# Performance work log

Measured on AMD Instinct MI355X. Metric: run time of the kernel, lower is better.

## Reference

```python
import jax, jax.numpy as jnp
import numpy as np

N, D = 131072, 512
G, NG = 512, 256  # G groups of equal size NG, contiguous; N == G*NG
MARGIN, LAMBDA_CD, LAMBDA_CDD, LAMBDA_PCC, K_MARGIN = 2.0, 0.0, 1.0, 1.0, 0.02
EPS = 1e-6


def setup_inputs() -> dict:
    key = jax.random.key(0)
    k1, k2, k3, k4 = jax.random.split(key, 4)
    z_r = jax.random.normal(k1, (N, D), jnp.float32)
    z_r = z_r / jnp.linalg.norm(z_r, axis=-1, keepdims=True)
    z_v = jax.random.normal(k2, (N, D), jnp.float32)
    z_v = z_v / jnp.linalg.norm(z_v, axis=-1, keepdims=True)
    labels = jax.random.randint(k3, (N,), 0, 2)
    groups = jnp.repeat(jnp.arange(G), NG)  # contiguous equal-size groups
    var_lens = jax.random.randint(k4, (N,), 0, 10000)
    return {"z_r": z_r, "z_v": z_v, "labels": labels, "groups": groups, "var_lens": var_lens}


def reference(z_r, z_v, labels, groups, var_lens):
    # cosine distance per pair: [N]
    d = 1.0 - jnp.sum(z_r * z_v, axis=-1)

    mb = (labels == 0).astype(d.dtype)
    mp = (labels == 1).astype(d.dtype)
    nb, npos = mb.sum(), mp.sum()
    db_mean = jnp.sum(d * mb) / jnp.maximum(nb, 1.0)
    dp_mean = jnp.sum(d * mp) / jnp.maximum(npos, 1.0)

    l_cd = jnp.where(nb > 0, db_mean, 0.0)
    l_cdd = jnp.where((nb > 0) & (npos > 0),
                      jax.nn.relu(MARGIN + db_mean - dp_mean), 0.0)

    # --- per-group losses, vectorized over G equal-size contiguous groups ---
    d_g = d.reshape(G, NG)                                   # [G, n_g]
    v_g = var_lens.reshape(G, NG).astype(d.dtype)            # [G, n_g]

    # Pearson-style z-score matching loss (torch std is unbiased, ddof=1)
    v_std = jnp.std(v_g, axis=1, ddof=1)
    d_std = jnp.std(d_g, axis=1, ddof=1)
    v_z = (v_g - v_g.mean(axis=1, keepdims=True)) / (v_std + EPS)[:, None]
    d_z = (d_g - d_g.mean(axis=1, keepdims=True)) / (d_std + EPS)[:, None]
    corr_loss = jnp.mean((v_z - d_z) ** 2, axis=1)
    corr_loss = jnp.where((v_std > 0) & (d_std > 0), corr_loss, 0.0)

    # sort each group by var_len
    order = jnp.argsort(v_g, axis=1)
    v_s = jnp.take_along_axis(v_g, order, axis=1)            # [G, n_g]
    d_s = jnp.take_along_axis(d_g, order, axis=1)            # [G, n_g]

    # neighbor monotonicity violation
    neigh_viol = jnp.mean(jax.nn.relu(d_s[:, :-1] - d_s[:, 1:] + K_MARGIN), axis=1)

    # pairwise rank loss: dv[g,i,j] = v_s[g,j] - v_s[g,i] (matches torch unsqueeze(0)-unsqueeze(1))
    dv = v_s[:, None, :] - v_s[:, :, None]                   # [G, n_g, n_g]
    dd = d_s[:, None, :] - d_s[:, :, None]                   # [G, n_g, n_g]
    mask = (dv > 0).astype(d.dtype)
    cnt = mask.sum(axis=(1, 2))
    pair_sum = jnp.sum(jax.nn.relu(K_MARGIN - dd) * mask, axis=(1, 2))
    rank_loss = jnp.where(cnt > 0, pair_sum / jnp.maximum(cnt, 1.0), 0.0)

    group_loss = corr_loss + neigh_viol + rank_loss          # [G]
    # size-weighted sum; all groups have equal size NG -> plain mean
    l_pcc = jnp.mean(group_loss)

    total = LAMBDA_CD * l_cd + LAMBDA_CDD * l_cdd + LAMBDA_PCC * l_pcc
    return total, l_cdd, l_pcc, d
```

## Files before the change

### kernel.cpp

```cpp
#include <hip/hip_runtime.h>

#define NTOT   131072
#define GCNT   512
#define NGRP   256
#define KMARG  0.02f
#define CMARG  2.0f
#define EPSC   1e-6f

typedef float f4 __attribute__((ext_vector_type(4)));

template <int NW, int M>
__device__ __forceinline__ void block_sum_m(float* v, float* red) {
  const int t = threadIdx.x;
#pragma unroll
  for (int m = 0; m < M; ++m) {
#pragma unroll
    for (int off = 32; off; off >>= 1) v[m] += __shfl_down(v[m], off, 64);
  }
  __syncthreads();
  if ((t & 63) == 0) {
#pragma unroll
    for (int m = 0; m < M; ++m) red[(t >> 6) * M + m] = v[m];
  }
  __syncthreads();
#pragma unroll
  for (int m = 0; m < M; ++m) {
    float s = 0.0f;
#pragma unroll
    for (int i = 0; i < NW; ++i) s += red[i * M + m];
    v[m] = s;
  }
}

__device__ __forceinline__ float wave_sum(float v) {
#pragma unroll
  for (int off = 32; off; off >>= 1) v += __shfl_down(v, off, 64);
  return v;
}

__global__ __launch_bounds__(256) void fused_kernel(const float* __restrict__ zr,
                                                    const float* __restrict__ zv,
                                                    const int* __restrict__ labels,
                                                    const int* __restrict__ varl,
                                                    float* __restrict__ dvec,
                                                    float* __restrict__ gout) {
  __shared__ float  red[4 * 4];
  __shared__ float  sd[NGRP];
  __shared__ float2 skv[NGRP];
  __shared__ float  sdat[NGRP];
  const int g = blockIdx.x, t = threadIdx.x;
  const int wave = t >> 6, lane = t & 63;
  const size_t rowbase = (size_t)g * NGRP;
  const int rot = (g * 74) & 255;

#define LOADRP(Adst, Bdst, rg_) do {                                       \
    const f4* rp_ = (const f4*)zr + ((rowbase + (size_t)(rg_)) << 7);      \
    const f4* vp_ = (const f4*)zv + ((rowbase + (size_t)(rg_)) << 7);      \
    Adst[0] = rp_[lane];       Bdst[0] = vp_[lane];                        \
    Adst[1] = rp_[lane + 64];  Bdst[1] = vp_[lane + 64];                   \
    Adst[2] = rp_[lane + 128]; Bdst[2] = vp_[lane + 128];                  \
    Adst[3] = rp_[lane + 192]; Bdst[3] = vp_[lane + 192];                  \
  } while (0)

#define CONSUME(A, B, rg_) do {                                            \
    f4 p_ = A[0] * B[0] + A[1] * B[1];                                     \
    f4 q_ = A[2] * B[2] + A[3] * B[3];                                     \
    float s0_ = wave_sum(p_.x + p_.y + p_.z + p_.w);                       \
    float s1_ = wave_sum(q_.x + q_.y + q_.z + q_.w);                       \
    if (lane == 0) {                                                       \
      const float d0_ = 1.0f - s0_, d1_ = 1.0f - s1_;                      \
      sd[(rg_)]     = d0_;                                                 \
      sd[(rg_) + 1] = d1_;                                                 \
      dvec[rowbase + (rg_)]     = d0_;                                     \
      dvec[rowbase + (rg_) + 1] = d1_;                                     \
    }                                                                      \
  } while (0)

  f4 Aa[4], Ba[4], Ab[4], Bb[4];
  int rg = ((wave << 1) + rot) & 255;
  LOADRP(Aa, Ba, rg);
#pragma unroll 1
  for (int it = 0; it < 16; ++it) {
    const int rgB = (rg + 8) & 255;
    LOADRP(Ab, Bb, rgB);
    CONSUME(Aa, Ba, rg);
    const int rgA = (rg + 16) & 255;
    if (it != 15) LOADRP(Aa, Ba, rgA);
    CONSUME(Ab, Bb, rgB);
    rg = rgA;
  }
  __syncthreads();

  const int idx = g * NGRP + t;
  const float dv  = sd[t];
  const float vv  = (float)varl[idx];
  const int   lab = labels[idx];

  skv[t] = make_float2(vv, dv);

  float sA[4] = {dv, vv, (lab == 0) ? dv : 0.0f, (lab == 0) ? 1.0f : 0.0f};
  block_sum_m<4, 4>(sA, red);
  const float sumd = sA[0], sumv = sA[1], sb = sA[2], cb = sA[3];
  const float md = sumd * (1.0f / NGRP), mv = sumv * (1.0f / NGRP);

  const float vdev = vv - mv, ddev = dv - md;
  float sB[3] = {vdev * vdev, ddev * ddev, vdev * ddev};
  block_sum_m<4, 3>(sB, red);
  const float svv = sB[0], sdd = sB[1], svd = sB[2];
  const float vstd = sqrtf(svv * (1.0f / (NGRP - 1)));
  const float dstd = sqrtf(sdd * (1.0f / (NGRP - 1)));
  const float iv = 1.0f / (vstd + EPSC), id = 1.0f / (dstd + EPSC);
  float corr = (svv * iv * iv + sdd * id * id - 2.0f * svd * iv * id) * (1.0f / NGRP);
  corr = (vstd > 0.0f && dstd > 0.0f) ? corr : 0.0f;

  int rank = 0;
  float pc = 0.0f, ps = 0.0f;
  const float pre = KMARG + dv;
  for (int j = 0; j < NGRP; ++j) {
    const float2 kv = skv[j];
    const float vj = kv.x, dj = kv.y;
    if (vj > vv) {
      pc += 1.0f;
      ps += fmaxf(pre - dj, 0.0f);
    }
    rank += (vj < vv || (vj == vv && j < t)) ? 1 : 0;
  }
  sdat[rank] = dv;
  __syncthreads();
  const float nv = (t < NGRP - 1) ? fmaxf(sdat[t] - sdat[t + 1] + KMARG, 0.0f) : 0.0f;

  float sC[3] = {ps, pc, nv};
  block_sum_m<4, 3>(sC, red);
  const float rank_loss = (sC[1] > 0.0f) ? sC[0] / fmaxf(sC[1], 1.0f) : 0.0f;
  const float neigh = sC[2] * (1.0f / (NGRP - 1));

  if (t == 0) {
    gout[g]            = corr + neigh + rank_loss;
    gout[GCNT + g]     = sb;
    gout[2 * GCNT + g] = cb;
    gout[3 * GCNT + g] = sumd;
  }
#undef LOADRP
#undef CONSUME
}

__global__ __launch_bounds__(512) void final_kernel(const float* __restrict__ gout,
                                                    float* __restrict__ out) {
  __shared__ float red[8 * 4];
  const int t = threadIdx.x;
  float s[4] = {gout[t], gout[GCNT + t], gout[2 * GCNT + t], gout[3 * GCNT + t]};
  block_sum_m<8, 4>(s, red);
  if (t == 0) {
    const float L = s[0], SB = s[1], CB = s[2], SumD = s[3];
    const float SP = SumD - SB;
    const float CP = (float)NTOT - CB;
    const float db = SB / fmaxf(CB, 1.0f);
    const float dp = SP / fmaxf(CP, 1.0f);
    const float l_cdd = (CB > 0.0f && CP > 0.0f) ? fmaxf(CMARG + db - dp, 0.0f) : 0.0f;
    const float l_pcc = L * (1.0f / GCNT);
    out[0] = l_cdd + l_pcc;
    out[1] = l_cdd;
    out[2] = l_pcc;
  }
}

extern "C" void kernel_launch(void* const* d_in, const int* in_sizes, int n_in,
                              void* d_out, int out_size, void* d_ws, size_t ws_size,
                              hipStream_t stream) {
  const float* zr     = (const float*)d_in[0];
  const float* zv     = (const float*)d_in[1];
  const int*   labels = (const int*)d_in[2];
  const int*   varl   = (const int*)d_in[4];
  float* out  = (float*)d_out;
  float* dvec = out + 3;
  float* gws  = (float*)d_ws;

  fused_kernel<<<GCNT, 256, 0, stream>>>(zr, zv, labels, varl, dvec, gws);
  final_kernel<<<1, 512, 0, stream>>>(gws, out);
}
```

Measured before the change: 128.4 us.

## Hand-schedule row loads with inline asm nontemporal loads and explicit waitcnt

```diff
diff --git a/kernel.cpp b/kernel.cpp
--- a/kernel.cpp
+++ b/kernel.cpp
@@ -8,6 +8,23 @@
 #define EPSC   1e-6f
 
 typedef float f4 __attribute__((ext_vector_type(4)));
+
+#define GLD4_NT(d0, d1, d2, d3, p)                                         \
+  asm volatile("global_load_dwordx4 %0, %4, off nt\n\t"                    \
+               "global_load_dwordx4 %1, %4, off offset:1024 nt\n\t"        \
+               "global_load_dwordx4 %2, %4, off offset:2048 nt\n\t"        \
+               "global_load_dwordx4 %3, %4, off offset:3072 nt"            \
+               : "=&v"(d0), "=&v"(d1), "=&v"(d2), "=&v"(d3) : "v"(p))
+#define GLD4_CA(d0, d1, d2, d3, p)                                         \
+  asm volatile("global_load_dwordx4 %0, %4, off\n\t"                       \
+               "global_load_dwordx4 %1, %4, off offset:1024\n\t"           \
+               "global_load_dwordx4 %2, %4, off offset:2048\n\t"           \
+               "global_load_dwordx4 %3, %4, off offset:3072"               \
+               : "=&v"(d0), "=&v"(d1), "=&v"(d2), "=&v"(d3) : "v"(p))
+#define WAIT8 do { asm volatile("s_waitcnt vmcnt(8)" ::: "memory");        \
+                   __builtin_amdgcn_sched_barrier(0); } while (0)
+#define WAIT0 do { asm volatile("s_waitcnt vmcnt(0)" ::: "memory");        \
+                   __builtin_amdgcn_sched_barrier(0); } while (0)
 
 template <int NW, int M>
 __device__ __forceinline__ void block_sum_m(float* v, float* red) {
@@ -51,45 +68,53 @@
   const int g = blockIdx.x, t = threadIdx.x;
   const int wave = t >> 6, lane = t & 63;
   const size_t rowbase = (size_t)g * NGRP;
-  const int rot = (g * 74) & 255;
-
-#define LOADRP(Adst, Bdst, rg_) do {                                       \
-    const f4* rp_ = (const f4*)zr + ((rowbase + (size_t)(rg_)) << 7);      \
-    const f4* vp_ = (const f4*)zv + ((rowbase + (size_t)(rg_)) << 7);      \
-    Adst[0] = rp_[lane];       Bdst[0] = vp_[lane];                        \
-    Adst[1] = rp_[lane + 64];  Bdst[1] = vp_[lane + 64];                   \
-    Adst[2] = rp_[lane + 128]; Bdst[2] = vp_[lane + 128];                  \
-    Adst[3] = rp_[lane + 192]; Bdst[3] = vp_[lane + 192];                  \
+  const f4* zr4 = (const f4*)zr;
+  const f4* zv4 = (const f4*)zv;
+
+#define ISSUE(k, R0, R1, R2, R3, V0, V1, V2, V3) do {                      \
+    const size_t row0_ = rowbase + (size_t)((k) * 8 + wave * 2);           \
+    const f4* pr_ = zr4 + (row0_ << 7) + lane;                             \
+    const f4* pv_ = zv4 + (row0_ << 7) + lane;                             \
+    GLD4_NT(R0, R1, R2, R3, pr_);                                          \
+    GLD4_CA(V0, V1, V2, V3, pv_);                                          \
   } while (0)
 
-#define CONSUME(A, B, rg_) do {                                            \
-    f4 p_ = A[0] * B[0] + A[1] * B[1];                                     \
-    f4 q_ = A[2] * B[2] + A[3] * B[3];                                     \
-    float s0_ = wave_sum(p_.x + p_.y + p_.z + p_.w);                       \
-    float s1_ = wave_sum(q_.x + q_.y + q_.z + q_.w);                       \
+#define CONSUME(k, R0, R1, R2, R3, V0, V1, V2, V3) do {                    \
+    f4 p_ = R0 * V0 + R1 * V1;                                             \
+    f4 q_ = R2 * V2 + R3 * V3;                                             \
+    float s0_ = wave_sum((p_.x + p_.y) + (p_.z + p_.w));                   \
+    float s1_ = wave_sum((q_.x + q_.y) + (q_.z + q_.w));                   \
+    const int rg_ = (k) * 8 + wave * 2;                                    \
     if (lane == 0) {                                                       \
-      const float d0_ = 1.0f - s0_, d1_ = 1.0f - s1_;                      \
-      sd[(rg_)]     = d0_;                                                 \
-      sd[(rg_) + 1] = d1_;                                                 \
-      dvec[rowbase + (rg_)]     = d0_;                                     \
-      dvec[rowbase + (rg_) + 1] = d1_;                                     \
+      sd[rg_]     = 1.0f - s0_;                                            \
+      sd[rg_ + 1] = 1.0f - s1_;                                            \
     }                                                                      \
   } while (0)
 
-  f4 Aa[4], Ba[4], Ab[4], Bb[4];
-  int rg = ((wave << 1) + rot) & 255;
-  LOADRP(Aa, Ba, rg);
+  f4 Ra0, Ra1, Ra2, Ra3, Va0, Va1, Va2, Va3;
+  f4 Rb0, Rb1, Rb2, Rb3, Vb0, Vb1, Vb2, Vb3;
+
+  ISSUE(0, Ra0, Ra1, Ra2, Ra3, Va0, Va1, Va2, Va3);
 #pragma unroll 1
-  for (int it = 0; it < 16; ++it) {
-    const int rgB = (rg + 8) & 255;
-    LOADRP(Ab, Bb, rgB);
-    CONSUME(Aa, Ba, rg);
-    const int rgA = (rg + 16) & 255;
-    if (it != 15) LOADRP(Aa, Ba, rgA);
-    CONSUME(Ab, Bb, rgB);
-    rg = rgA;
-  }
-  __syncthreads();
+  for (int kk = 0; kk < 15; ++kk) {
+    const int k = 2 * kk;
+    ISSUE(k + 1, Rb0, Rb1, Rb2, Rb3, Vb0, Vb1, Vb2, Vb3);
+    WAIT8;
+    CONSUME(k, Ra0, Ra1, Ra2, Ra3, Va0, Va1, Va2, Va3);
+    ISSUE(k + 2, Ra0, Ra1, Ra2, Ra3, Va0, Va1, Va2, Va3);
+    WAIT8;
+    CONSUME(k + 1, Rb0, Rb1, Rb2, Rb3, Vb0, Vb1, Vb2, Vb3);
+  }
+  ISSUE(31, Rb0, Rb1, Rb2, Rb3, Vb0, Vb1, Vb2, Vb3);
+  WAIT8;
+  CONSUME(30, Ra0, Ra1, Ra2, Ra3, Va0, Va1, Va2, Va3);
+  WAIT0;
+  CONSUME(31, Rb0, Rb1, Rb2, Rb3, Vb0, Vb1, Vb2, Vb3);
+#undef ISSUE
+#undef CONSUME
+  __syncthreads();
+
+  __builtin_nontemporal_store(sd[t], dvec + rowbase + t);
 
   const int idx = g * NGRP + t;
   const float dv  = sd[t];
@@ -140,8 +165,6 @@
     gout[2 * GCNT + g] = cb;
     gout[3 * GCNT + g] = sumd;
   }
-#undef LOADRP
-#undef CONSUME
 }
 
 __global__ __launch_bounds__(512) void final_kernel(const float* __restrict__ gout,
```

New measurement: 114.3 us. 1.12x faster.
